# Performance work log

Measured on AMD Instinct MI355X. Metric: run time of the kernel, lower is better.

Reference implementation:

```python
import jax, jax.numpy as jnp
import numpy as np

TAU = 0.01          # init_temperature
N_CODEWORDS = 512
EPS = 1e-10


def setup_inputs() -> dict:
    key = jax.random.key(0)
    k1, k2, k3 = jax.random.split(key, 3)
    B, C, H, W = 8, 256, 64, 64
    K = N_CODEWORDS
    feats = jax.random.normal(k1, (B, C, H, W), dtype=jnp.float32)
    codebook = jax.random.normal(k2, (K, C), dtype=jnp.float32)
    # standard Gumbel(0,1) noise, matching torch's F.gumbel_softmax sampling
    gumbel_noise = jax.random.gumbel(k3, (B, H * W, K), dtype=jnp.float32)
    return {"feats": feats, "codebook": codebook, "gumbel_noise": gumbel_noise}


def reference(feats, codebook, gumbel_noise):
    B, C, H, W = feats.shape
    K = codebook.shape[0]
    N = H * W
    # (B, C, H, W) -> (B, N, C) tokens
    f = feats.reshape(B, C, N).transpose(0, 2, 1)
    # affinity[b,n,k] = ((f[b,n,:] - cb[k,:]).sum(-1))**2
    # sum over channels commutes with the subtraction, so reduce first
    # instead of materializing the (B, N, K, C) broadcast the torch code builds.
    sf = f.sum(axis=-1)            # (B, N)
    sw = codebook.sum(axis=-1)     # (K,)
    affinity = (sf[:, :, None] - sw[None, None, :]) ** 2   # (B, N, K)
    logits = jnp.exp(-affinity)
    # gumbel-softmax (soft, hard=False), tau = TAU, over codeword axis
    soft_one_hot = jax.nn.softmax((logits + gumbel_noise) / TAU, axis=2)
    qy = jax.nn.softmax(logits, axis=2)
    kld_loss = jnp.sum(qy * jnp.log(qy * K + EPS), axis=2).mean()
    codewords = jnp.argmax(soft_one_hot, axis=2).reshape(B, H, W)
    # weighted codeword sum: (B, N, K) @ (K, C) -> (B, N, C)
    sel = jnp.einsum("bnk,kc->bnc", soft_one_hot, codebook)
    sel_codewords = sel.transpose(0, 2, 1).reshape(B, C, H, W)
    mat_id_probs = soft_one_hot.transpose(0, 2, 1).reshape(B, K, H, W)
    return (sel_codewords, codewords, kld_loss, mat_id_probs)
```

## Files before the change

kernel.cpp:

```cpp
#include <hip/hip_runtime.h>
#include <math.h>

#define NB  8
#define NC  256
#define NHW 4096
#define NK  512
#define TOK 64

#define OFF_SEL 0ULL
#define OFF_CW  8388608ULL
#define OFF_KLD 8421376ULL
#define OFF_MAT 8421377ULL

#define SM_PTILE 0
#define SM_SW    33792
#define SM_SF    37888
#define SM_KCNT  38400
#define SM_KLIST 38656
#define SM_WLIST 42752
#define SM_KLD   46848
#define SM_TOTAL 46976


__global__ void gumbel_prep(const float* __restrict__ cb, double* __restrict__ ws) {
    const int l = threadIdx.x & 63;
    const int w = threadIdx.x >> 6;
    const int k = blockIdx.x * 4 + w;
    const float4 v = *reinterpret_cast<const float4*>(cb + (size_t)k * NC + l * 4);
    double s = (double)v.x + (double)v.y + (double)v.z + (double)v.w;
    #pragma unroll
    for (int off = 32; off > 0; off >>= 1) s += __shfl_xor(s, off);
    if (l == 0) ws[k] = s;
    if (blockIdx.x == 0 && threadIdx.x == 0) ws[NK] = 0.0;
}

__global__ void __launch_bounds__(1024, 4)
gumbel_main(const float* __restrict__ feats, const float* __restrict__ gumbel,
            const float* __restrict__ cb, double* __restrict__ ws,
            float* __restrict__ out) {
    extern __shared__ char smem[];
    unsigned char* p_tile = reinterpret_cast<unsigned char*>(smem + SM_PTILE);
    double* sw_lds = reinterpret_cast<double*>(smem + SM_SW);
    double* part   = reinterpret_cast<double*>(smem + SM_PTILE);
    double* sf_lds = reinterpret_cast<double*>(smem + SM_SF);
    int*    kcnt   = reinterpret_cast<int*>(smem + SM_KCNT);
    int*    klist  = reinterpret_cast<int*>(smem + SM_KLIST);
    float*  wlist  = reinterpret_cast<float*>(smem + SM_WLIST);
    double* kldp   = reinterpret_cast<double*>(smem + SM_KLD);

    const int tid = threadIdx.x;
    const int t   = tid & 63;
    const int grp = tid >> 6;
    const int b   = blockIdx.x >> 6;
    const int n0  = (blockIdx.x & 63) * TOK;

    {
        const float* fp = feats + ((size_t)b * NC + grp * 16) * NHW + n0 + t;
        double s = 0.0;
        #pragma unroll
        for (int i = 0; i < 16; ++i) s += (double)fp[(size_t)i * NHW];
        part[grp * 64 + t] = s;
    }
    if (tid < NK) sw_lds[tid] = ws[tid];
    __syncthreads();
    if (tid < TOK) {
        double acc = 0.0;
        #pragma unroll
        for (int i = 0; i < 16; ++i) acc += part[i * 64 + t];
        sf_lds[t] = acc;
        kcnt[t] = 0;
    }
    __syncthreads();

    double kld_wave = 0.0;
    for (int tt = grp * 4; tt < grp * 4 + 4; ++tt) {
        const double sf_t = sf_lds[tt];
        const float* gp = gumbel + ((size_t)(b * NHW + n0 + tt)) * NK;
        float y[8], gg[8];
        float ym = -1.0e30f; int kb = 0;
        float E = 0.f, T1 = 0.f;
        #pragma unroll
        for (int j2 = 0; j2 < 4; ++j2) {
            const float2 g2 = reinterpret_cast<const float2*>(gp)[t + 64 * j2];
            #pragma unroll
            for (int q = 0; q < 2; ++q) {
                const int k = 2 * t + 128 * j2 + q;
                const float g = q ? g2.y : g2.x;
                const float d = (float)(sf_t - sw_lds[k]);
                const float logit = __expf(-d * d);
                const float yy = logit + g;
                y[j2 * 2 + q] = yy; gg[j2 * 2 + q] = g;
                const float el = __expf(logit);
                E += el; T1 += logit * el;
                if (yy > ym) { ym = yy; kb = k; }
            }
        }
        #pragma unroll
        for (int off = 32; off > 0; off >>= 1) {
            const float oy = __shfl_xor(ym, off);
            const int   ok = __shfl_xor(kb, off);
            if (oy > ym || (oy == ym && ok < kb)) { ym = oy; kb = ok; }
        }
        float ys = -1.0e30f;
        #pragma unroll
        for (int j = 0; j < 8; ++j) {
            const int k = 2 * t + 128 * (j >> 1) + (j & 1);
            if (k != kb) ys = fmaxf(ys, y[j]);
        }
        #pragma unroll
        for (int off = 32; off > 0; off >>= 1) ys = fmaxf(ys, __shfl_xor(ys, off));
        if (ym - ys < 1e-4f) {
            double ym64 = -1.0e300; int kb64 = 0;
            #pragma unroll
            for (int j = 0; j < 8; ++j) {
                const int k = 2 * t + 128 * (j >> 1) + (j & 1);
                const double dd = sf_t - sw_lds[k];
                const double aff = dd * dd;
                const double logit = (aff < 45.0) ? exp(-aff) : 0.0;
                const double yy = logit + (double)gg[j];
                if (yy > ym64) { ym64 = yy; kb64 = k; }
            }
            #pragma unroll
            for (int off = 32; off > 0; off >>= 1) {
                const double oy = __shfl_xor(ym64, off);
                const int    ok = __shfl_xor(kb64, off);
                if (oy > ym64 || (oy == ym64 && ok < kb64)) { ym64 = oy; kb64 = ok; }
            }
            kb = kb64;
        }
        #pragma unroll
        for (int off = 32; off > 0; off >>= 1) { E += __shfl_xor(E, off); T1 += __shfl_xor(T1, off); }
        float S = 0.f; float pr[8];
        #pragma unroll
        for (int j = 0; j < 8; ++j) {
            const float p = __expf((y[j] - ym) * 100.0f);
            pr[j] = p; S += p;
        }
        #pragma unroll
        for (int off = 32; off > 0; off >>= 1) S += __shfl_xor(S, off);
        const float inv = 1.0f / S;
        if (t == 0) {
            out[OFF_CW + (size_t)b * NHW + n0 + tt] = (float)kb;
            kld_wave += (double)(T1 / E + 6.2383246250395075f - logf(E));
        }
        #pragma unroll
        for (int j = 0; j < 8; ++j) {
            const int k = 2 * t + 128 * (j >> 1) + (j & 1);
            const float w = pr[j] * inv;
            p_tile[k * 66 + tt] = (unsigned char)(w * 255.0f + 0.5f);
            if (w > 1e-7f) {
                const int idx = atomicAdd(&kcnt[tt], 1);
                if (idx < 16) { klist[tt * 16 + idx] = k; wlist[tt * 16 + idx] = w; }
            }
        }
    }
    if (t == 0) kldp[grp] = kld_wave;
    __syncthreads();
    if (tid == 0) {
        double acc = 0.0;
        #pragma unroll
        for (int i = 0; i < 16; ++i) acc += kldp[i];
        atomicAdd(&ws[NK], acc);
    }

    {
        const size_t base = OFF_MAT + (size_t)b * NK * NHW + n0 + t;
        #pragma unroll
        for (int pass = 0; pass < 32; ++pass) {
            const int k = pass * 16 + grp;
            out[base + (size_t)k * NHW] = (float)p_tile[k * 66 + t] * (1.0f / 255.0f);
        }
    }

    {
        const int cnt = min(kcnt[t], 16);
        float acc[16];
        #pragma unroll
        for (int i = 0; i < 16; ++i) acc[i] = 0.f;
        for (int e = 0; e < cnt; ++e) {
            const int k = klist[t * 16 + e];
            const float wgt = wlist[t * 16 + e];
            const float4* cr = reinterpret_cast<const float4*>(cb + (size_t)k * NC + grp * 16);
            #pragma unroll
            for (int q = 0; q < 4; ++q) {
                const float4 v = cr[q];
                acc[q * 4 + 0] += wgt * v.x; acc[q * 4 + 1] += wgt * v.y;
                acc[q * 4 + 2] += wgt * v.z; acc[q * 4 + 3] += wgt * v.w;
            }
        }
        const size_t base = OFF_SEL + ((size_t)b * NC + grp * 16) * NHW + n0 + t;
        #pragma unroll
        for (int i = 0; i < 16; ++i) out[base + (size_t)i * NHW] = acc[i];
    }
}

__global__ void gumbel_fin(const double* __restrict__ ws, float* __restrict__ out) {
    out[OFF_KLD] = (float)(ws[NK] * (1.0 / 32768.0));
}

extern "C" void kernel_launch(void* const* d_in, const int* in_sizes, int n_in,
                              void* d_out, int out_size, void* d_ws, size_t ws_size,
                              hipStream_t stream) {
    const float* feats = (const float*)d_in[0];
    const float* cb    = (const float*)d_in[1];
    const float* gum   = (const float*)d_in[2];
    double* ws = (double*)d_ws;
    float* out = (float*)d_out;
    gumbel_prep<<<128, 256, 0, stream>>>(cb, ws);
    gumbel_main<<<512, 1024, SM_TOTAL, stream>>>(feats, gum, cb, ws, out);
    gumbel_fin<<<1, 1, 0, stream>>>(ws, out);
}
```

Measured before the change: 63.15 us.

## Split main kernel into token pass and separate transposed probability writer

The token kernel now writes quantized 8-bit probabilities row-major to a workspace buffer. A new gs_mat kernel then transposes them through LDS and writes the (B,K,H,W) probability output with wide contiguous nontemporal stores, replacing the in-block byte tile. Gumbel loads are widened to float4, and the softmax exponentials are computed locally before the cross-lane max and then rescaled. This adds an extra launch and a 16 MB workspace round trip, and keeps the old monolithic kernel as a fallback when the workspace is too small.

```diff
diff --git a/kernel.cpp b/kernel.cpp
--- a/kernel.cpp
+++ b/kernel.cpp
@@ -1,26 +1,19 @@
 #include <hip/hip_runtime.h>
 #include <math.h>
+#include <stdint.h>
 
 #define NB  8
 #define NC  256
 #define NHW 4096
 #define NK  512
-#define TOK 64
 
 #define OFF_SEL 0ULL
 #define OFF_CW  8388608ULL
 #define OFF_KLD 8421376ULL
 #define OFF_MAT 8421377ULL
 
-#define SM_PTILE 0
-#define SM_SW    33792
-#define SM_SF    37888
-#define SM_KCNT  38400
-#define SM_KLIST 38656
-#define SM_WLIST 42752
-#define SM_KLD   46848
-#define SM_TOTAL 46976
-
+#define WS_WSP_OFF 8192ULL
+#define WS_NEED    (WS_WSP_OFF + (size_t)NB * NHW * NK)
 
 __global__ void gumbel_prep(const float* __restrict__ cb, double* __restrict__ ws) {
     const int l = threadIdx.x & 63;
@@ -34,47 +27,241 @@
     if (blockIdx.x == 0 && threadIdx.x == 0) ws[NK] = 0.0;
 }
 
-__global__ void __launch_bounds__(1024, 4)
-gumbel_main(const float* __restrict__ feats, const float* __restrict__ gumbel,
-            const float* __restrict__ cb, double* __restrict__ ws,
-            float* __restrict__ out) {
-    extern __shared__ char smem[];
-    unsigned char* p_tile = reinterpret_cast<unsigned char*>(smem + SM_PTILE);
-    double* sw_lds = reinterpret_cast<double*>(smem + SM_SW);
-    double* part   = reinterpret_cast<double*>(smem + SM_PTILE);
-    double* sf_lds = reinterpret_cast<double*>(smem + SM_SF);
-    int*    kcnt   = reinterpret_cast<int*>(smem + SM_KCNT);
-    int*    klist  = reinterpret_cast<int*>(smem + SM_KLIST);
-    float*  wlist  = reinterpret_cast<float*>(smem + SM_WLIST);
-    double* kldp   = reinterpret_cast<double*>(smem + SM_KLD);
+__global__ void __launch_bounds__(1024)
+gs_token(const float* __restrict__ feats, const float* __restrict__ gumbel,
+         const float* __restrict__ cb, double* __restrict__ ws,
+         unsigned char* __restrict__ wsp, float* __restrict__ out) {
+    __shared__ double sw_s[NK];
+    __shared__ double part[16][64];
+    __shared__ double sf_s[64];
+    __shared__ int    kcnt[64];
+    __shared__ int    klist[64][16];
+    __shared__ float  wlist[64][16];
+    __shared__ double kldp[16];
+
+    const int tid = threadIdx.x;
+    const int l   = tid & 63;
+    const int w   = tid >> 6;
+    const int b   = blockIdx.x >> 6;
+    const int n0  = (blockIdx.x & 63) * 64;
+
+    {
+        const float* fp = feats + ((size_t)b * NC + w * 16) * NHW + n0 + l;
+        double s = 0.0;
+        #pragma unroll
+        for (int i = 0; i < 16; ++i) s += (double)fp[(size_t)i * NHW];
+        part[w][l] = s;
+    }
+    if (tid < NK) sw_s[tid] = ws[tid];
+    __syncthreads();
+    if (tid < 64) {
+        double acc = 0.0;
+        #pragma unroll
+        for (int i = 0; i < 16; ++i) acc += part[i][tid];
+        sf_s[tid] = acc;
+        kcnt[tid] = 0;
+    }
+    __syncthreads();
+
+    double kld_wave = 0.0;
+    for (int tt = w * 4; tt < w * 4 + 4; ++tt) {
+        const double sf_t = sf_s[tt];
+        const float* gp = gumbel + ((size_t)(b * NHW + n0 + tt)) * NK;
+        float y[8], gg[8];
+        float ymloc = -1.0e30f; int kbloc = 0;
+        float E = 0.f, T1 = 0.f;
+        #pragma unroll
+        for (int j4 = 0; j4 < 2; ++j4) {
+            const float4 g4 = reinterpret_cast<const float4*>(gp)[l + 64 * j4];
+            #pragma unroll
+            for (int q = 0; q < 4; ++q) {
+                const int k = 4 * l + 256 * j4 + q;
+                const float g = (q == 0) ? g4.x : (q == 1) ? g4.y : (q == 2) ? g4.z : g4.w;
+                const float d = (float)(sf_t - sw_s[k]);
+                const float logit = __expf(-d * d);
+                const float yy = logit + g;
+                y[j4 * 4 + q] = yy; gg[j4 * 4 + q] = g;
+                const float el = __expf(logit);
+                E += el; T1 += logit * el;
+                if (yy > ymloc) { ymloc = yy; kbloc = k; }
+            }
+        }
+        float Sloc = 0.f; float prloc[8];
+        #pragma unroll
+        for (int j = 0; j < 8; ++j) {
+            const float p = __expf((y[j] - ymloc) * 100.0f);
+            prloc[j] = p; Sloc += p;
+        }
+        float ym = ymloc; int kb = kbloc;
+        #pragma unroll
+        for (int off = 32; off > 0; off >>= 1) {
+            const float oy = __shfl_xor(ym, off);
+            const int   ok = __shfl_xor(kb, off);
+            if (oy > ym || (oy == ym && ok < kb)) { ym = oy; kb = ok; }
+        }
+        float ys = -1.0e30f;
+        #pragma unroll
+        for (int j = 0; j < 8; ++j) {
+            const int k = 4 * l + 256 * (j >> 2) + (j & 3);
+            if (k != kb) ys = fmaxf(ys, y[j]);
+        }
+        #pragma unroll
+        for (int off = 32; off > 0; off >>= 1) ys = fmaxf(ys, __shfl_xor(ys, off));
+        if (ym - ys < 1e-4f) {
+            double ym64 = -1.0e300; int kb64 = 0;
+            #pragma unroll
+            for (int j = 0; j < 8; ++j) {
+                const int k = 4 * l + 256 * (j >> 2) + (j & 3);
+                const double dd = sf_t - sw_s[k];
+                const double aff = dd * dd;
+                const double logit = (aff < 45.0) ? exp(-aff) : 0.0;
+                const double yy = logit + (double)gg[j];
+                if (yy > ym64) { ym64 = yy; kb64 = k; }
+            }
+            #pragma unroll
+            for (int off = 32; off > 0; off >>= 1) {
+                const double oy = __shfl_xor(ym64, off);
+                const int    ok = __shfl_xor(kb64, off);
+                if (oy > ym64 || (oy == ym64 && ok < kb64)) { ym64 = oy; kb64 = ok; }
+            }
+            kb = kb64;
+        }
+        const float c = __expf((ymloc - ym) * 100.0f);
+        float S = Sloc * c;
+        #pragma unroll
+        for (int off = 32; off > 0; off >>= 1) {
+            E += __shfl_xor(E, off); T1 += __shfl_xor(T1, off); S += __shfl_xor(S, off);
+        }
+        const float inv = 1.0f / S;
+        if (l == 0) {
+            out[OFF_CW + (size_t)b * NHW + n0 + tt] = (float)kb;
+            kld_wave += (double)(T1 / E + 6.2383246250395075f - logf(E));
+        }
+        uint32_t* wrow = reinterpret_cast<uint32_t*>(wsp + (((size_t)(b * NHW + n0 + tt)) << 9));
+        #pragma unroll
+        for (int j4 = 0; j4 < 2; ++j4) {
+            uint32_t pk = 0;
+            #pragma unroll
+            for (int q = 0; q < 4; ++q) {
+                const int j = j4 * 4 + q;
+                const float wgt = prloc[j] * c * inv;
+                pk |= ((uint32_t)(wgt * 255.0f + 0.5f)) << (8 * q);
+                if (wgt > 1e-7f) {
+                    const int k = 4 * l + 256 * j4 + q;
+                    const int idx = atomicAdd(&kcnt[tt], 1);
+                    if (idx < 16) { klist[tt][idx] = k; wlist[tt][idx] = wgt; }
+                }
+            }
+            wrow[l + 64 * j4] = pk;
+        }
+    }
+    if (l == 0) kldp[w] = kld_wave;
+    __syncthreads();
+    if (tid == 0) {
+        double acc = 0.0;
+        #pragma unroll
+        for (int i = 0; i < 16; ++i) acc += kldp[i];
+        atomicAdd(&ws[NK], acc);
+    }
+
+    {
+        const int cnt = min(kcnt[l], 16);
+        float acc[16];
+        #pragma unroll
+        for (int i = 0; i < 16; ++i) acc[i] = 0.f;
+        for (int e = 0; e < cnt; ++e) {
+            const int k = klist[l][e];
+            const float wgt = wlist[l][e];
+            const float4* cr = reinterpret_cast<const float4*>(cb + (size_t)k * NC + w * 16);
+            #pragma unroll
+            for (int q = 0; q < 4; ++q) {
+                const float4 v = cr[q];
+                acc[q * 4 + 0] += wgt * v.x; acc[q * 4 + 1] += wgt * v.y;
+                acc[q * 4 + 2] += wgt * v.z; acc[q * 4 + 3] += wgt * v.w;
+            }
+        }
+        float* base = out + OFF_SEL + ((size_t)b * NC + w * 16) * NHW + n0 + l;
+        #pragma unroll
+        for (int i = 0; i < 16; ++i)
+            __builtin_nontemporal_store(acc[i], base + (size_t)i * NHW);
+    }
+}
+
+__global__ void __launch_bounds__(1024)
+gs_mat(const unsigned char* __restrict__ wsp, float* __restrict__ out) {
+    extern __shared__ unsigned char lbs[];
+    const int tid = threadIdx.x;
+    const int bid = blockIdx.x;
+    const int b   = bid >> 5;
+    const int nch = (bid >> 2) & 7;
+    const int kch = bid & 3;
+
+    const uint32_t* wp32 = reinterpret_cast<const uint32_t*>(wsp);
+    #pragma unroll
+    for (int it = 0; it < 16; ++it) {
+        const int di  = tid + 1024 * it;
+        const int row = di >> 5;
+        const int dw  = di & 31;
+        const uint32_t v = wp32[((size_t)(b * NHW + nch * 512 + row) << 7) + kch * 32 + dw];
+        *reinterpret_cast<uint32_t*>(lbs + row * 132 + dw * 4) = v;
+    }
+    __syncthreads();
+
+    const int l = tid & 63, w = tid >> 6;
+    #pragma unroll
+    for (int m = 0; m < 8; ++m) {
+        const int kk = w * 8 + m;
+        const int k  = kch * 128 + kk;
+        float* base = out + OFF_MAT + ((size_t)b * NK + k) * NHW + nch * 512;
+        #pragma unroll
+        for (int j = 0; j < 8; ++j) {
+            const int nl = l + 64 * j;
+            const float f = (float)lbs[nl * 132 + kk] * (1.0f / 255.0f);
+            __builtin_nontemporal_store(f, base + nl);
+        }
+    }
+}
+
+__global__ void __launch_bounds__(1024)
+gs_mono(const float* __restrict__ feats, const float* __restrict__ gumbel,
+        const float* __restrict__ cb, double* __restrict__ ws,
+        float* __restrict__ out) {
+    __shared__ unsigned char p_tile[NK * 66];
+    __shared__ double sw_s[NK];
+    __shared__ double part[16][64];
+    __shared__ double sf_s[64];
+    __shared__ int    kcnt[64];
+    __shared__ int    klist[64][16];
+    __shared__ float  wlist[64][16];
+    __shared__ double kldp[16];
 
     const int tid = threadIdx.x;
     const int t   = tid & 63;
     const int grp = tid >> 6;
     const int b   = blockIdx.x >> 6;
-    const int n0  = (blockIdx.x & 63) * TOK;
+    const int n0  = (blockIdx.x & 63) * 64;
 
     {
         const float* fp = feats + ((size_t)b * NC + grp * 16) * NHW + n0 + t;
         double s = 0.0;
         #pragma unroll
         for (int i = 0; i < 16; ++i) s += (double)fp[(size_t)i * NHW];
-        part[grp * 64 + t] = s;
-    }
-    if (tid < NK) sw_lds[tid] = ws[tid];
-    __syncthreads();
-    if (tid < TOK) {
+        part[grp][t] = s;
+    }
+    if (tid < NK) sw_s[tid] = ws[tid];
+    __syncthreads();
+    if (tid < 64) {
         double acc = 0.0;
         #pragma unroll
-        for (int i = 0; i < 16; ++i) acc += part[i * 64 + t];
-        sf_lds[t] = acc;
-        kcnt[t] = 0;
+        for (int i = 0; i < 16; ++i) acc += part[i][tid];
+        sf_s[tid] = acc;
+        kcnt[tid] = 0;
     }
     __syncthreads();
 
     double kld_wave = 0.0;
     for (int tt = grp * 4; tt < grp * 4 + 4; ++tt) {
-        const double sf_t = sf_lds[tt];
+        const double sf_t = sf_s[tt];
         const float* gp = gumbel + ((size_t)(b * NHW + n0 + tt)) * NK;
         float y[8], gg[8];
         float ym = -1.0e30f; int kb = 0;
@@ -86,7 +273,7 @@
             for (int q = 0; q < 2; ++q) {
                 const int k = 2 * t + 128 * j2 + q;
                 const float g = q ? g2.y : g2.x;
-                const float d = (float)(sf_t - sw_lds[k]);
+                const float d = (float)(sf_t - sw_s[k]);
                 const float logit = __expf(-d * d);
                 const float yy = logit + g;
                 y[j2 * 2 + q] = yy; gg[j2 * 2 + q] = g;
@@ -114,7 +301,7 @@
             #pragma unroll
             for (int j = 0; j < 8; ++j) {
                 const int k = 2 * t + 128 * (j >> 1) + (j & 1);
-                const double dd = sf_t - sw_lds[k];
+                const double dd = sf_t - sw_s[k];
                 const double aff = dd * dd;
                 const double logit = (aff < 45.0) ? exp(-aff) : 0.0;
                 const double yy = logit + (double)gg[j];
@@ -146,11 +333,11 @@
         #pragma unroll
         for (int j = 0; j < 8; ++j) {
             const int k = 2 * t + 128 * (j >> 1) + (j & 1);
-            const float w = pr[j] * inv;
-            p_tile[k * 66 + tt] = (unsigned char)(w * 255.0f + 0.5f);
-            if (w > 1e-7f) {
+            const float wv = pr[j] * inv;
+            p_tile[k * 66 + tt] = (unsigned char)(wv * 255.0f + 0.5f);
+            if (wv > 1e-7f) {
                 const int idx = atomicAdd(&kcnt[tt], 1);
-                if (idx < 16) { klist[tt * 16 + idx] = k; wlist[tt * 16 + idx] = w; }
+                if (idx < 16) { klist[tt][idx] = k; wlist[tt][idx] = wv; }
             }
         }
     }
@@ -162,7 +349,6 @@
         for (int i = 0; i < 16; ++i) acc += kldp[i];
         atomicAdd(&ws[NK], acc);
     }
-
     {
         const size_t base = OFF_MAT + (size_t)b * NK * NHW + n0 + t;
         #pragma unroll
@@ -171,15 +357,14 @@
             out[base + (size_t)k * NHW] = (float)p_tile[k * 66 + t] * (1.0f / 255.0f);
         }
     }
-
     {
         const int cnt = min(kcnt[t], 16);
         float acc[16];
         #pragma unroll
         for (int i = 0; i < 16; ++i) acc[i] = 0.f;
         for (int e = 0; e < cnt; ++e) {
-            const int k = klist[t * 16 + e];
-            const float wgt = wlist[t * 16 + e];
+            const int k = klist[t][e];
+            const float wgt = wlist[t][e];
             const float4* cr = reinterpret_cast<const float4*>(cb + (size_t)k * NC + grp * 16);
             #pragma unroll
             for (int q = 0; q < 4; ++q) {
@@ -207,6 +392,14 @@
     double* ws = (double*)d_ws;
     float* out = (float*)d_out;
     gumbel_prep<<<128, 256, 0, stream>>>(cb, ws);
-    gumbel_main<<<512, 1024, SM_TOTAL, stream>>>(feats, gum, cb, ws, out);
+    if (ws_size >= WS_NEED) {
+        unsigned char* wsp = (unsigned char*)d_ws + WS_WSP_OFF;
+        (void)hipFuncSetAttribute(reinterpret_cast<const void*>(gs_mat),
+                                  hipFuncAttributeMaxDynamicSharedMemorySize, 512 * 132);
+        gs_token<<<512, 1024, 0, stream>>>(feats, gum, cb, ws, wsp, out);
+        gs_mat<<<256, 1024, 512 * 132, stream>>>(wsp, out);
+    } else {
+        gs_mono<<<512, 1024, 0, stream>>>(feats, gum, cb, ws, out);
+    }
     gumbel_fin<<<1, 1, 0, stream>>>(ws, out);
 }
```

New measurement: 80.16 us. 1.27x slower.
